# Kernel optimization log

Hardware: AMD Instinct MI355X
Metric: run time of the kernel (lower is better)

The kernel has to match this reference:

```python
import jax, jax.numpy as jnp
import numpy as np

B, T, I = 256, 384, 32      # batch, seq_len, input_size
M, D, O = 128, 64, 128      # ring positions, embedding_dim, num_outputs
K = 2                       # attention_radius -> 2K+1 = 5 neighbors
TEMP = 8.0                  # attention_temperature
EPS = 1e-5                  # torch LayerNorm default eps


def setup_inputs() -> dict:
    key = jax.random.key(0)
    ks = jax.random.split(key, 12)
    def lin(kw, kb, fan_in, shape_w, shape_b):
        lim = 1.0 / np.sqrt(fan_in)
        W = jax.random.uniform(kw, shape_w, jnp.float32, -lim, lim)
        b = jax.random.uniform(kb, shape_b, jnp.float32, -lim, lim)
        return W, b
    Wp, bp = lin(ks[0], ks[1], I, (I, D), (D,))
    Wg, bg = lin(ks[2], ks[3], D, (D, 1), (1,))
    Wo, bo = lin(ks[4], ks[5], D, (D, O), (O,))
    return {
        "x": jax.random.normal(ks[6], (B, T, I), jnp.float32),
        "ptr_init": jax.random.uniform(ks[7], (B,), jnp.float32) * M,
        "Wp": Wp, "bp": bp,
        "gamma": jnp.ones((D,), jnp.float32),
        "beta": jnp.zeros((D,), jnp.float32),
        "jump_dest": jax.random.uniform(ks[8], (M,), jnp.float32) * M,
        "Wg": Wg, "bg": bg,
        "ctx_strength": jnp.asarray(0.2, jnp.float32),
        "Wo": Wo, "bo": bo,
    }


def reference(x, ptr_init, Wp, bp, gamma, beta, jump_dest, Wg, bg, ctx_strength, Wo, bo):
    offsets = jnp.arange(-K, K + 1)               # [2K+1]
    bidx = jnp.arange(B)[:, None]                 # [B,1] batch index for gather/scatter
    half = M / 2.0
    ctx_scale = jax.nn.sigmoid(ctx_strength)

    def step(carry, x_t):
        ring, hidden, ptr = carry                 # [B,M,D], [B,D], [B]
        emb = jnp.tanh(x_t @ Wp + bp)             # input projection + activation
        # Gaussian attention over circular neighborhood of floor(ptr)
        base = jnp.clip(jnp.floor(ptr).astype(jnp.int32), 0, M - 1)
        idx = (base[:, None] + offsets[None, :]) % M            # [B,2K+1]
        delta = jnp.mod(idx.astype(ptr.dtype) - ptr[:, None] + half, M) - half
        w = jax.nn.softmax(-(delta ** 2) / TEMP, axis=1)        # [B,2K+1]
        neigh = ring[bidx, idx]                                  # gather [B,2K+1,D]
        ctx = jnp.sum(w[:, :, None] * neigh, axis=1)             # [B,D]
        state = jnp.tanh(emb + ctx_scale * ctx + hidden)
        # LayerNorm (biased variance, affine)
        mu = jnp.mean(state, axis=-1, keepdims=True)
        var = jnp.var(state, axis=-1, keepdims=True)
        hidden_new = (state - mu) * jax.lax.rsqrt(var + EPS) * gamma + beta
        # scatter-add weighted state back into the ring
        ring = ring.at[bidx, idx].add(w[:, :, None] * state[:, None, :])
        # pointer update: hard STE gate between learned jump and +1 walk
        cur = jnp.clip(ptr.astype(jnp.int32), 0, M - 1)
        jump_target = jump_dest[cur]
        jl = (state @ Wg + bg)[:, 0]
        probs = jax.nn.sigmoid(jl)
        gate = (probs > 0.5).astype(state.dtype) - jax.lax.stop_gradient(probs) + probs
        walk = (ptr + 1.0) % M
        ptr_new = jnp.where(gate > 0.5, jump_target, walk)
        return (ring, hidden_new, ptr_new), None

    ring0 = jnp.zeros((B, M, D), x.dtype)
    h0 = jnp.zeros((B, D), x.dtype)
    (ring, hidden, ptr), _ = jax.lax.scan(step, (ring0, h0, ptr_init), jnp.swapaxes(x, 0, 1))
    logits = hidden @ Wo + bo                     # [B, O]
    return logits
```

## Files before the change

### kernel.cpp

```cpp
#include <hip/hip_runtime.h>
#include <hip/hip_bf16.h>


#define BB 256
#define TT 384
#define II 32
#define MM 128
#define DD 64
#define OO 128
#define K2 0.1803368801f
#define PR 132
#define CHK 32
#define NCHK (TT / CHK)
#define NSLOT 3

__device__ __forceinline__ float bfbits(unsigned int lo16) {
    return __uint_as_float(lo16 << 16);
}
__device__ __forceinline__ float ldf(const void* p, long long i, bool isbf) {
    if (isbf) return bfbits((unsigned int)((const unsigned short*)p)[i]);
    return ((const float*)p)[i];
}

template <int CTRL>
__device__ __forceinline__ float dpp_add(float x) {
    int s = __builtin_amdgcn_update_dpp(0, __float_as_int(x), CTRL, 0xf, 0xf, true);
    return x + __int_as_float(s);
}
__device__ __forceinline__ void reduce3(float& a, float& b, float& c) {
    a = dpp_add<0x111>(a); b = dpp_add<0x111>(b); c = dpp_add<0x111>(c);
    a = dpp_add<0x112>(a); b = dpp_add<0x112>(b); c = dpp_add<0x112>(c);
    a = dpp_add<0x114>(a); b = dpp_add<0x114>(b); c = dpp_add<0x114>(c);
    a = dpp_add<0x118>(a); b = dpp_add<0x118>(b); c = dpp_add<0x118>(c);
    a = dpp_add<0x142>(a); b = dpp_add<0x142>(b); c = dpp_add<0x142>(c);
    a = dpp_add<0x143>(a); b = dpp_add<0x143>(b); c = dpp_add<0x143>(c);
    a = __int_as_float(__builtin_amdgcn_readlane(__float_as_int(a), 63));
    b = __int_as_float(__builtin_amdgcn_readlane(__float_as_int(b), 63));
    c = __int_as_float(__builtin_amdgcn_readlane(__float_as_int(c), 63));
}

__device__ __forceinline__ float fast_tanh(float x) {
    float e = __builtin_amdgcn_exp2f(x * 2.885390082f);
    return fmaf(-2.0f, __builtin_amdgcn_rcpf(e + 1.0f), 1.0f);
}

__global__ __launch_bounds__(256, 1)
void ring_fused(const void* __restrict__ x,
                const void* __restrict__ ptr_init,
                const void* __restrict__ Wp,
                const void* __restrict__ bp,
                const void* __restrict__ gamma,
                const void* __restrict__ beta,
                const void* __restrict__ jump_dest,
                const void* __restrict__ Wg,
                const void* __restrict__ bg,
                const void* __restrict__ cs,
                const void* __restrict__ Wo,
                const void* __restrict__ bo,
                void* __restrict__ out)
{
    __shared__ float ring[PR * DD];
    __shared__ float ebuf[NSLOT * CHK * DD];
    __shared__ float tab[MM * 8];
    __shared__ float hsh[DD];
    __shared__ int chunk_ready[NCHK];
    __shared__ int cons_done;

    const int tid = threadIdx.x;
    const int wid = tid >> 6;
    const int lane = tid & 63;
    const int b = blockIdx.x;
    const bool isbf = (((const unsigned int*)gamma)[0] == 0x3f803f80u);

    if (tid < NCHK) chunk_ready[tid] = 0;
    if (tid == 0) cons_done = 0;
    __syncthreads();

    if (wid != 0) {
        float wp[II];
        #pragma unroll
        for (int k = 0; k < II; k++) wp[k] = ldf(Wp, k * DD + lane, isbf);
        const float bpv = ldf(bp, lane, isbf);
        volatile int* vcd = &cons_done;

        for (int c = wid - 1; c < NCHK; c += 3) {
            while (*vcd < c - 2) __builtin_amdgcn_s_sleep(16);
            const int slot = c % NSLOT;
            float* eslot = ebuf + slot * (CHK * DD);
            for (int k = 0; k < CHK; k++) {
                const size_t t = (size_t)c * CHK + k;
                float acc = bpv;
                if (isbf) {
                    const uint4* xr = (const uint4*)
                        ((const unsigned short*)x + ((size_t)b * TT + t) * II);
                    #pragma unroll
                    for (int q = 0; q < 4; q++) {
                        uint4 u = xr[q];
                        unsigned int uu[4] = {u.x, u.y, u.z, u.w};
                        #pragma unroll
                        for (int e = 0; e < 4; e++) {
                            acc = fmaf(bfbits(uu[e] & 0xffffu), wp[q * 8 + e * 2], acc);
                            acc = fmaf(bfbits(uu[e] >> 16),     wp[q * 8 + e * 2 + 1], acc);
                        }
                    }
                } else {
                    const float4* xr = (const float4*)
                        ((const float*)x + ((size_t)b * TT + t) * II);
                    #pragma unroll
                    for (int q = 0; q < II / 4; q++) {
                        float4 v = xr[q];
                        acc = fmaf(v.x, wp[q * 4 + 0], acc);
                        acc = fmaf(v.y, wp[q * 4 + 1], acc);
                        acc = fmaf(v.z, wp[q * 4 + 2], acc);
                        acc = fmaf(v.w, wp[q * 4 + 3], acc);
                    }
                }
                eslot[k * DD + lane] = fast_tanh(acc);
            }
            __threadfence_block();
            if (lane == 0) *(volatile int*)&chunk_ready[c] = 1;
        }
        return;
    }

    {
        float4 z4 = make_float4(0.f, 0.f, 0.f, 0.f);
        #pragma unroll
        for (int i = 0; i < (PR * DD) / (4 * 64); i++)
            ((float4*)ring)[lane + i * 64] = z4;
    }

    const float gam = ldf(gamma, lane, isbf);
    const float bet = ldf(beta, lane, isbf);
    const float wgv = ldf(Wg, lane, isbf);
    const float bgv = ldf(bg, 0, isbf);
    const float csv = 1.0f / (1.0f + expf(-ldf(cs, 0, isbf)));

    #pragma unroll
    for (int h = 0; h < 2; h++) {
        const int m = lane + h * 64;
        const float jd = ldf(jump_dest, m, isbf);
        int bj = (int)jd; bj = min(bj, MM - 1);
        const float fj = jd - (float)bj;
        float e[5], se = 0.0f;
        #pragma unroll
        for (int j = 0; j < 5; j++) {
            const float dd = (float)(j - 2) - fj;
            e[j] = __builtin_amdgcn_exp2f(dd * dd * -K2);
            se += e[j];
        }
        const float inv = __builtin_amdgcn_rcpf(se);
        #pragma unroll
        for (int j = 0; j < 5; j++) tab[m * 8 + j] = e[j] * inv;
        tab[m * 8 + 5] = __int_as_float(bj);
    }

    const float p0 = ldf(ptr_init, b, isbf);
    int sbase = __builtin_amdgcn_readfirstlane(min(max((int)floorf(p0), 0), MM - 1));
    const float frac = p0 - (float)sbase;
    float w0, w1, w2, w3, w4;
    {
        float e[5], se = 0.0f;
        #pragma unroll
        for (int j = 0; j < 5; j++) {
            const float dd = (float)(j - 2) - frac;
            e[j] = __builtin_amdgcn_exp2f(dd * dd * -K2);
            se += e[j];
        }
        const float inv = __builtin_amdgcn_rcpf(se);
        w0 = e[0] * inv; w1 = e[1] * inv; w2 = e[2] * inv;
        w3 = e[3] * inv; w4 = e[4] * inv;
    }

    float hid = 0.0f;
    volatile int* vcr = chunk_ready;

    for (int c = 0; c < NCHK; c++) {
        while (!vcr[c]) __builtin_amdgcn_s_sleep(2);
        const float* eslot = ebuf + (c % NSLOT) * (CHK * DD);

        #pragma unroll 8
        for (int k = 0; k < CHK; k++) {
            const float ecv = eslot[k * DD + lane];
            const float* ce = tab + (sbase << 3);
            const float c0 = ce[0], c1 = ce[1], c2 = ce[2], c3 = ce[3], c4 = ce[4];
            const int bjc = __float_as_int(ce[5]);

            float* rb = ring + sbase * DD + lane;
            const float nb0 = rb[0 * DD], nb1 = rb[1 * DD], nb2 = rb[2 * DD],
                        nb3 = rb[3 * DD], nb4 = rb[4 * DD];

            const float ctx = fmaf(w0, nb0, fmaf(w1, nb1, 0.0f)) +
                              fmaf(w2, nb2, fmaf(w3, nb3, w4 * nb4));
            const float snn = fast_tanh(fmaf(csv, ctx, ecv + hid));

            float r0 = snn, r1 = snn * snn, r2 = snn * wgv;
            reduce3(r0, r1, r2);

            const float nv0 = fmaf(w0, snn, nb0), nv1 = fmaf(w1, snn, nb1),
                        nv2 = fmaf(w2, snn, nb2), nv3 = fmaf(w3, snn, nb3),
                        nv4 = fmaf(w4, snn, nb4);
            rb[0 * DD] = nv0; rb[1 * DD] = nv1; rb[2 * DD] = nv2;
            rb[3 * DD] = nv3; rb[4 * DD] = nv4;
            if (sbase <= 3 || sbase >= MM - 4) {
                const float nv[5] = {nv0, nv1, nv2, nv3, nv4};
                #pragma unroll
                for (int j = 0; j < 5; j++) {
                    const int p = sbase + j;
                    if (p < 4)        ring[(p + MM) * DD + lane] = nv[j];
                    else if (p >= MM) ring[(p - MM) * DD + lane] = nv[j];
                }
            }

            const float mu = r0 * (1.0f / 64.0f);
            const float var = fmaf(-mu, mu, r1 * (1.0f / 64.0f));
            const float rstd = __builtin_amdgcn_rsqf(var + 1e-5f);
            hid = fmaf((snn - mu) * rstd, gam, bet);

            const float jl = r2 + bgv;
            const bool jump = __builtin_amdgcn_readfirstlane(__float_as_int(jl)) > 0;
            sbase = __builtin_amdgcn_readfirstlane(jump ? bjc : ((sbase + 1) & (MM - 1)));
            w0 = jump ? c0 : w0; w1 = jump ? c1 : w1; w2 = jump ? c2 : w2;
            w3 = jump ? c3 : w3; w4 = jump ? c4 : w4;
        }
        if (lane == 0) *(volatile int*)&cons_done = c + 1;
    }

    hsh[lane] = hid;
    float a0 = ldf(bo, lane, isbf);
    float a1 = ldf(bo, lane + 64, isbf);
    #pragma unroll 8
    for (int d = 0; d < DD; d++) {
        const float h = hsh[d];
        a0 = fmaf(h, ldf(Wo, d * OO + lane, isbf), a0);
        a1 = fmaf(h, ldf(Wo, d * OO + lane + 64, isbf), a1);
    }
    if (isbf) {
        __hip_bfloat16* o = (__hip_bfloat16*)out;
        o[(size_t)b * OO + lane] = __float2bfloat16(a0);
        o[(size_t)b * OO + lane + 64] = __float2bfloat16(a1);
    } else {
        float* o = (float*)out;
        o[(size_t)b * OO + lane] = a0;
        o[(size_t)b * OO + lane + 64] = a1;
    }
}

extern "C" void kernel_launch(void* const* d_in, const int* in_sizes, int n_in,
                              void* d_out, int out_size, void* d_ws, size_t ws_size,
                              hipStream_t stream) {
    ring_fused<<<BB, 256, 0, stream>>>(
        d_in[0], d_in[1], d_in[2], d_in[3], d_in[4], d_in[5],
        d_in[6], d_in[7], d_in[8], d_in[9], d_in[10], d_in[11], d_out);
}
```

Measured before the change: 199.7 us.

## Prefetch next-step ring neighbours and jump-table entries off the serial recurrence chain

The consumer wave now keeps the five ring neighbours in registers. It loads both possible next windows (the walk window's new sixth row and the jump target's five rows) plus the next table entry before the current step's reduction, then selects with the jump bit. This removes the LDS load latency from the step-to-step dependency chain. It also forwards freshly written values when the jump window overlaps the current window, widens the ring padding to 133 rows, and batch-loads eight embeddings at a time. The cost is extra LDS reads per step and more complex aliasing logic that must exactly match the scatter semantics.

```diff
diff --git a/kernel.cpp b/kernel.cpp
--- a/kernel.cpp
+++ b/kernel.cpp
@@ -9,7 +9,7 @@
 #define DD 64
 #define OO 128
 #define K2 0.1803368801f
-#define PR 132
+#define PR 133
 #define CHK 32
 #define NCHK (TT / CHK)
 #define NSLOT 3
@@ -85,8 +85,7 @@
 
         for (int c = wid - 1; c < NCHK; c += 3) {
             while (*vcd < c - 2) __builtin_amdgcn_s_sleep(16);
-            const int slot = c % NSLOT;
-            float* eslot = ebuf + slot * (CHK * DD);
+            float* eslot = ebuf + (c % NSLOT) * (CHK * DD);
             for (int k = 0; k < CHK; k++) {
                 const size_t t = (size_t)c * CHK + k;
                 float acc = bpv;
@@ -126,8 +125,9 @@
     {
         float4 z4 = make_float4(0.f, 0.f, 0.f, 0.f);
         #pragma unroll
-        for (int i = 0; i < (PR * DD) / (4 * 64); i++)
+        for (int i = 0; i < 33; i++)
             ((float4*)ring)[lane + i * 64] = z4;
+        ring[8448 + lane] = 0.0f;
     }
 
     const float gam = ldf(gamma, lane, isbf);
@@ -172,56 +172,87 @@
         w3 = e[3] * inv; w4 = e[4] * inv;
     }
 
+    const float* te = tab + (sbase << 3);
+    float c0 = te[0], c1 = te[1], c2 = te[2], c3 = te[3], c4 = te[4];
+    int bjc = __float_as_int(te[5]);
+    float nb0 = 0.f, nb1 = 0.f, nb2 = 0.f, nb3 = 0.f, nb4 = 0.f;
     float hid = 0.0f;
+
     volatile int* vcr = chunk_ready;
 
     for (int c = 0; c < NCHK; c++) {
         while (!vcr[c]) __builtin_amdgcn_s_sleep(2);
         const float* eslot = ebuf + (c % NSLOT) * (CHK * DD);
 
-        #pragma unroll 8
-        for (int k = 0; k < CHK; k++) {
-            const float ecv = eslot[k * DD + lane];
-            const float* ce = tab + (sbase << 3);
-            const float c0 = ce[0], c1 = ce[1], c2 = ce[2], c3 = ce[3], c4 = ce[4];
-            const int bjc = __float_as_int(ce[5]);
-
-            float* rb = ring + sbase * DD + lane;
-            const float nb0 = rb[0 * DD], nb1 = rb[1 * DD], nb2 = rb[2 * DD],
-                        nb3 = rb[3 * DD], nb4 = rb[4 * DD];
-
-            const float ctx = fmaf(w0, nb0, fmaf(w1, nb1, 0.0f)) +
-                              fmaf(w2, nb2, fmaf(w3, nb3, w4 * nb4));
-            const float snn = fast_tanh(fmaf(csv, ctx, ecv + hid));
-
-            float r0 = snn, r1 = snn * snn, r2 = snn * wgv;
-            reduce3(r0, r1, r2);
-
-            const float nv0 = fmaf(w0, snn, nb0), nv1 = fmaf(w1, snn, nb1),
-                        nv2 = fmaf(w2, snn, nb2), nv3 = fmaf(w3, snn, nb3),
-                        nv4 = fmaf(w4, snn, nb4);
-            rb[0 * DD] = nv0; rb[1 * DD] = nv1; rb[2 * DD] = nv2;
-            rb[3 * DD] = nv3; rb[4 * DD] = nv4;
-            if (sbase <= 3 || sbase >= MM - 4) {
-                const float nv[5] = {nv0, nv1, nv2, nv3, nv4};
-                #pragma unroll
-                for (int j = 0; j < 5; j++) {
-                    const int p = sbase + j;
-                    if (p < 4)        ring[(p + MM) * DD + lane] = nv[j];
-                    else if (p >= MM) ring[(p - MM) * DD + lane] = nv[j];
+        for (int k8 = 0; k8 < CHK; k8 += 8) {
+            float ev[8];
+            #pragma unroll
+            for (int j = 0; j < 8; j++) ev[j] = eslot[(k8 + j) * DD + lane];
+
+            #pragma unroll
+            for (int k = 0; k < 8; k++) {
+                const float* rb = ring + sbase * DD + lane;
+                const float W4p = rb[5 * DD];
+                const float* rj = ring + bjc * DD + lane;
+                float pj[5];
+                pj[0] = rj[0 * DD]; pj[1] = rj[1 * DD]; pj[2] = rj[2 * DD];
+                pj[3] = rj[3 * DD]; pj[4] = rj[4 * DD];
+
+                const float ctx = fmaf(w0, nb0, fmaf(w1, nb1, 0.0f)) +
+                                  fmaf(w2, nb2, fmaf(w3, nb3, w4 * nb4));
+                const float snn = fast_tanh(fmaf(csv, ctx, ev[k] + hid));
+
+                float r0 = snn, r1 = snn * snn, r2 = snn * wgv;
+                reduce3(r0, r1, r2);
+
+                const float nv0 = fmaf(w0, snn, nb0), nv1 = fmaf(w1, snn, nb1),
+                            nv2 = fmaf(w2, snn, nb2), nv3 = fmaf(w3, snn, nb3),
+                            nv4 = fmaf(w4, snn, nb4);
+                float* rw = ring + sbase * DD + lane;
+                rw[0 * DD] = nv0; rw[1 * DD] = nv1; rw[2 * DD] = nv2;
+                rw[3 * DD] = nv3; rw[4 * DD] = nv4;
+                if (sbase <= 4 || sbase >= MM - 4) {
+                    const float nvv[5] = {nv0, nv1, nv2, nv3, nv4};
+                    #pragma unroll
+                    for (int j = 0; j < 5; j++) {
+                        const int p = sbase + j;
+                        if (p < 5)        ring[(p + MM) * DD + lane] = nvv[j];
+                        else if (p >= MM) ring[(p - MM) * DD + lane] = nvv[j];
+                    }
                 }
+
+                const int s = (bjc - sbase) & (MM - 1);
+                if (s <= 4 || s >= MM - 4) {
+                    const float nvv[5] = {nv0, nv1, nv2, nv3, nv4};
+                    #pragma unroll
+                    for (int j = 0; j < 5; j++) {
+                        const int kk = (s + j) & (MM - 1);
+                        if (kk <= 4) pj[j] = nvv[kk];
+                    }
+                }
+
+                const float mu = r0 * (1.0f / 64.0f);
+                const float var = fmaf(-mu, mu, r1 * (1.0f / 64.0f));
+                const float rstd = __builtin_amdgcn_rsqf(var + 1e-5f);
+                hid = fmaf((snn - mu) * rstd, gam, bet);
+
+                const float jl = r2 + bgv;
+                const bool jump =
+                    __builtin_amdgcn_readfirstlane(__float_as_int(jl)) > 0;
+                nb0 = jump ? pj[0] : nv1;
+                nb1 = jump ? pj[1] : nv2;
+                nb2 = jump ? pj[2] : nv3;
+                nb3 = jump ? pj[3] : nv4;
+                nb4 = jump ? pj[4] : W4p;
+                w0 = jump ? c0 : w0; w1 = jump ? c1 : w1; w2 = jump ? c2 : w2;
+                w3 = jump ? c3 : w3; w4 = jump ? c4 : w4;
+                sbase = __builtin_amdgcn_readfirstlane(
+                    jump ? bjc : ((sbase + 1) & (MM - 1)));
+
+                const float* t2 = tab + (sbase << 3);
+                c0 = t2[0]; c1 = t2[1]; c2 = t2[2]; c3 = t2[3]; c4 = t2[4];
+                bjc = __float_as_int(t2[5]);
             }
-
-            const float mu = r0 * (1.0f / 64.0f);
-            const float var = fmaf(-mu, mu, r1 * (1.0f / 64.0f));
-            const float rstd = __builtin_amdgcn_rsqf(var + 1e-5f);
-            hid = fmaf((snn - mu) * rstd, gam, bet);
-
-            const float jl = r2 + bgv;
-            const bool jump = __builtin_amdgcn_readfirstlane(__float_as_int(jl)) > 0;
-            sbase = __builtin_amdgcn_readfirstlane(jump ? bjc : ((sbase + 1) & (MM - 1)));
-            w0 = jump ? c0 : w0; w1 = jump ? c1 : w1; w2 = jump ? c2 : w2;
-            w3 = jump ? c3 : w3; w4 = jump ? c4 : w4;
         }
         if (lane == 0) *(volatile int*)&cons_done = c + 1;
     }
```

Result: no change. 203.3 us (+1.8%).
